# Kernel optimization log

Hardware: AMD Instinct MI355X
Metric: run time of the kernel (lower is better)

## Reference

```python
import jax, jax.numpy as jnp
import numpy as np

EMBED_DIM = 1024
NUM_HEADS = 16
HEAD_DIM = EMBED_DIM // NUM_HEADS
SCALE = HEAD_DIM ** -0.5
EPS = 1e-5


def _layer_norm(x, w, b):
    mu = jnp.mean(x, axis=-1, keepdims=True)
    var = jnp.mean(jnp.square(x - mu), axis=-1, keepdims=True)
    return (x - mu) * jax.lax.rsqrt(var + EPS) * w + b


def setup_inputs() -> dict:
    key = jax.random.key(0)
    ks = jax.random.split(key, 8)
    B, L, Lp, C = 8, 4096, 256, EMBED_DIM
    gain = 0.05  # xavier_uniform gain
    lim = gain * np.sqrt(6.0 / (C + C))
    return {
        "prompt": jax.random.normal(ks[0], (B, Lp, C), jnp.float32),
        "x": jax.random.normal(ks[1], (B, L, C), jnp.float32),
        "ln_q_w": jnp.ones((C,), jnp.float32),
        "ln_q_b": jnp.zeros((C,), jnp.float32),
        "ln_k_w": jnp.ones((C,), jnp.float32),
        "ln_k_b": jnp.zeros((C,), jnp.float32),
        "Wq": jax.random.uniform(ks[2], (C, C), jnp.float32, -lim, lim),
        "bq": jnp.zeros((C,), jnp.float32),
        "Wk": jax.random.uniform(ks[3], (C, C), jnp.float32, -lim, lim),
        "bk": jnp.zeros((C,), jnp.float32),
        "Wo": jax.random.uniform(ks[4], (C, C), jnp.float32, -lim, lim),
        "bo": jnp.zeros((C,), jnp.float32),
        "alpha": jnp.asarray(0.5, jnp.float32),
    }


def reference(prompt, x, ln_q_w, ln_q_b, ln_k_w, ln_k_b, Wq, bq, Wk, bk, Wo, bo, alpha):
    B, L, C = x.shape
    Lp = prompt.shape[1]
    H, D = NUM_HEADS, HEAD_DIM

    q = _layer_norm(prompt, ln_q_w, ln_q_b)
    k = _layer_norm(x, ln_k_w, ln_k_b)

    # torch Linear: y = x @ W^T + b (W is [out, in])
    Q = (q @ Wq.T + bq).reshape(B, Lp, H, D).transpose(0, 2, 1, 3)  # [B,H,Lp,D]
    K = (k @ Wk.T + bk).reshape(B, L, H, D).transpose(0, 2, 1, 3)   # [B,H,L,D]
    V = x.reshape(B, L, H, D).transpose(0, 2, 1, 3)                  # [B,H,L,D]

    Q = jnp.clip(Q, -10.0, 10.0)
    K = jnp.clip(K, -10.0, 10.0)

    scores = jnp.einsum('bhqd,bhkd->bhqk', Q, K) * SCALE
    scores = scores - jax.lax.stop_gradient(jnp.max(scores, axis=-1, keepdims=True))
    attn = jax.nn.softmax(scores, axis=-1)

    attn_out = jnp.einsum('bhqk,bhkd->bhqd', attn, V)
    attn_out = attn_out.transpose(0, 2, 1, 3).reshape(B, Lp, C)
    attn_out = attn_out @ Wo.T + bo

    global_signal = jnp.mean(attn_out, axis=1, keepdims=True)  # [B,1,C]
    a = jax.nn.sigmoid(alpha) * 0.3
    return x + a * global_signal
```

## Files before the change

### kernel.cpp

```cpp
#include <hip/hip_runtime.h>

typedef __attribute__((ext_vector_type(8))) short  short8;
typedef __attribute__((ext_vector_type(4))) float  floatx4;
typedef __attribute__((ext_vector_type(2))) unsigned int uint2v;

#define NS 8

__device__ __forceinline__ unsigned short f2b(float f) {
  union { float f; unsigned u; } c; c.f = f;
  unsigned r = c.u + 0x7FFFu + ((c.u >> 16) & 1u);
  return (unsigned short)(r >> 16);
}

__device__ __forceinline__ float b2f(unsigned short u) {
  union { unsigned u; float f; } c; c.u = (unsigned)u << 16;
  return c.f;
}

__device__ __forceinline__ unsigned cvt_pk_bf16(float a, float b) {
  unsigned r;
  asm("v_cvt_pk_bf16_f32 %0, %1, %2" : "=v"(r) : "v"(a), "v"(b));
  return r;
}

__device__ __forceinline__ void async_copy16(const void* g, void* l) {
  __builtin_amdgcn_global_load_lds(
      (const __attribute__((address_space(1))) void*)g,
      (__attribute__((address_space(3))) void*)l, 16, 0, 0);
}

__global__ __launch_bounds__(256) void ln_bf16_kernel(
    const float* __restrict__ src, const float* __restrict__ w,
    const float* __restrict__ bias, unsigned short* __restrict__ dst) {
  const size_t row = blockIdx.x;
  const int t = threadIdx.x;
  const float4 v = *(const float4*)&src[row * 1024 + t * 4];
  float s = v.x + v.y + v.z + v.w;
  float q = v.x * v.x + v.y * v.y + v.z * v.z + v.w * v.w;
#pragma unroll
  for (int m = 32; m >= 1; m >>= 1) {
    s += __shfl_xor(s, m, 64);
    q += __shfl_xor(q, m, 64);
  }
  __shared__ float ss[4], sq[4];
  if ((t & 63) == 0) { ss[t >> 6] = s; sq[t >> 6] = q; }
  __syncthreads();
  s = ss[0] + ss[1] + ss[2] + ss[3];
  q = sq[0] + sq[1] + sq[2] + sq[3];
  const float mu = s * (1.f / 1024.f);
  const float var = q * (1.f / 1024.f) - mu * mu;
  const float rs = rsqrtf(var + 1e-5f);
  const float4 wv = *(const float4*)&w[t * 4];
  const float4 bv = *(const float4*)&bias[t * 4];
  ushort4 o;
  o.x = f2b((v.x - mu) * rs * wv.x + bv.x);
  o.y = f2b((v.y - mu) * rs * wv.y + bv.y);
  o.z = f2b((v.z - mu) * rs * wv.z + bv.z);
  o.w = f2b((v.w - mu) * rs * wv.w + bv.w);
  *(ushort4*)&dst[row * 1024 + t * 4] = o;
}

__global__ __launch_bounds__(256) void conv_bf16_kernel(
    const float* __restrict__ src, unsigned short* __restrict__ dst) {
  const size_t i = (size_t)blockIdx.x * 256 + threadIdx.x;
  const float4 v = ((const float4*)src)[i];
  ushort4 o;
  o.x = f2b(v.x); o.y = f2b(v.y); o.z = f2b(v.z); o.w = f2b(v.w);
  ((ushort4*)dst)[i] = o;
}

__global__ __launch_bounds__(256) void vtrans_kernel(
    const float* __restrict__ x, unsigned short* __restrict__ Vbf) {
  const int bh = blockIdx.x, kb = blockIdx.y;
  const int b = bh >> 4, h = bh & 15;
  const int t = threadIdx.x;
  const int d = t >> 2, kc = t & 3;
  const float* xp = x + (size_t)(b * 4096 + kb * 256) * 1024 + h * 64 + d;
  unsigned short* vp = Vbf + ((size_t)bh * 64 + d) * 4096 + kb * 256;
#pragma unroll
  for (int c = 0; c < 8; c++) {
    const int kk = c * 32 + kc * 8;
    short8 o;
#pragma unroll
    for (int j = 0; j < 8; j++)
      o[j] = (short)f2b(xp[(size_t)(kk + j) * 1024]);
    *(short8*)&vp[kk] = o;
  }
}

__global__ __launch_bounds__(256) void gemm_bt_kernel(
    const unsigned short* __restrict__ A, const unsigned short* __restrict__ W,
    const float* __restrict__ bias, unsigned short* __restrict__ out, int M) {
  __shared__ __align__(16) unsigned short smem[2][128 * 64];
  unsigned short* As = smem[0];
  unsigned short* Bs = smem[1];
  const int tid = threadIdx.x;
  const int wave = tid >> 6, lane = tid & 63;
  const int quad = lane >> 4, l16 = lane & 15;
  const int id = blockIdx.x;
  const size_t m0 = (size_t)(id >> 3) * 128;
  const int n0 = (id & 7) * 128;
  const int wm = (wave >> 1) * 64, wn = (wave & 1) * 64;
  const int r8 = lane >> 3, cvv = lane & 7;
  const int csrc = cvv ^ r8;

  floatx4 acc[4][4];
#pragma unroll
  for (int i = 0; i < 4; i++)
#pragma unroll
    for (int j = 0; j < 4; j++) acc[i][j] = (floatx4){0.f, 0.f, 0.f, 0.f};

  const unsigned short* gA = A + (m0 + wave * 32 + r8) * 1024 + csrc * 8;
  const unsigned short* gB = W + ((size_t)(n0 + wave * 32 + r8)) * 1024 + csrc * 8;

  for (int k0 = 0; k0 < 1024; k0 += 64) {
    __syncthreads();
#pragma unroll
    for (int it = 0; it < 4; ++it) {
      async_copy16(gA + (size_t)it * 8 * 1024 + k0, &As[(wave * 4 + it) * 512]);
      async_copy16(gB + (size_t)it * 8 * 1024 + k0, &Bs[(wave * 4 + it) * 512]);
    }
    __syncthreads();
#pragma unroll
    for (int kh = 0; kh < 2; ++kh) {
      short8 af[4], bf[4];
#pragma unroll
      for (int mi = 0; mi < 4; mi++) {
        int row = wm + mi * 16 + l16;
        af[mi] = *(const short8*)&As[row * 64 + (((kh * 4 + quad) ^ (row & 7)) * 8)];
      }
#pragma unroll
      for (int ni = 0; ni < 4; ni++) {
        int row = wn + ni * 16 + l16;
        bf[ni] = *(const short8*)&Bs[row * 64 + (((kh * 4 + quad) ^ (row & 7)) * 8)];
      }
#pragma unroll
      for (int mi = 0; mi < 4; mi++)
#pragma unroll
        for (int ni = 0; ni < 4; ni++)
          acc[mi][ni] = __builtin_amdgcn_mfma_f32_16x16x32_bf16(af[mi], bf[ni], acc[mi][ni], 0, 0, 0);
    }
  }

  __syncthreads();
  unsigned short* Cs = smem[0];
#pragma unroll
  for (int ni = 0; ni < 4; ni++) {
    int n = n0 + wn + ni * 16 + l16;
    float bv = bias[n];
    int c = wn + ni * 16 + l16;
#pragma unroll
    for (int mi = 0; mi < 4; mi++)
#pragma unroll
      for (int p = 0; p < 4; p++) {
        int r = wm + mi * 16 + quad * 4 + p;
        float v = acc[mi][ni][p] + bv;
        v = fminf(10.f, fmaxf(-10.f, v));
        int cc = c >> 3;
        Cs[r * 128 + ((cc ^ (r & 7)) * 8) + (c & 7)] = f2b(v);
      }
  }
  __syncthreads();
#pragma unroll
  for (int i = 0; i < 8; ++i) {
    int r = (tid >> 4) + 16 * i;
    int cc = tid & 15;
    short8 v = *(const short8*)&Cs[r * 128 + ((cc ^ (r & 7)) * 8)];
    *(short8*)&out[(m0 + r) * 1024 + n0 + cc * 8] = v;
  }
}

__global__ __launch_bounds__(256) void attn_kernel(
    const unsigned short* __restrict__ Qp,
    const unsigned short* __restrict__ Kp,
    const unsigned short* __restrict__ Vbf,
    unsigned short* __restrict__ Onum,
    float* __restrict__ lpart) {
  const int bh = blockIdx.x, split = blockIdx.y;
  const int b = bh >> 4, h = bh & 15;
  const int tid = threadIdx.x, wave = tid >> 6, lane = tid & 63;
  const int quad = lane >> 4, l16 = lane & 15;
  const int r8 = lane >> 3, cvv = lane & 7, csrc = cvv ^ r8;

  __shared__ __align__(16) unsigned short smem[16384];
  unsigned short* Ks = smem;
  unsigned short* Vs = smem + 4096;
  unsigned short* Pw = smem + 8192;

  short8 qf[4][2];
#pragma unroll
  for (int mi = 0; mi < 4; mi++)
#pragma unroll
    for (int kh = 0; kh < 2; kh++)
      qf[mi][kh] = *(const short8*)&Qp[(size_t)(b * 256 + wave * 64 + mi * 16 + l16) * 1024 +
                                       h * 64 + kh * 32 + quad * 8];

  floatx4 oacc[4][4];
  floatx4 lacc[4];
#pragma unroll
  for (int i = 0; i < 4; i++) {
    lacc[i] = (floatx4){0.f, 0.f, 0.f, 0.f};
#pragma unroll
    for (int j = 0; j < 4; j++) oacc[i][j] = (floatx4){0.f, 0.f, 0.f, 0.f};
  }
  short8 ones;
#pragma unroll
  for (int j = 0; j < 8; j++) ones[j] = (short)0x3F80;

  const int kbase = split * (4096 / NS);
  const int rowbase = (wave & 1) * 32;
  const bool isK = (wave < 2);
  const unsigned short* gK = Kp + ((size_t)(b * 4096 + kbase + rowbase + r8)) * 1024 +
                             h * 64 + csrc * 8;
  const unsigned short* gV = Vbf + ((size_t)(bh * 64 + rowbase + r8)) * 4096 +
                             kbase + csrc * 8;

  const int T = 4096 / NS / 64;
  unsigned short* Pb = Pw + wave * 2048;

  uint4 stg[4];
  if (isK) {
#pragma unroll
    for (int it = 0; it < 4; ++it)
      stg[it] = *(const uint4*)&gK[((size_t)it * 8) * 1024];
  } else {
#pragma unroll
    for (int it = 0; it < 4; ++it)
      stg[it] = *(const uint4*)&gV[(size_t)it * 8 * 4096];
  }

  for (int t = 0; t < T; ++t) {
    __syncthreads();
    if (isK) {
#pragma unroll
      for (int it = 0; it < 4; ++it)
        *(uint4*)((char*)Ks + (rowbase + it * 8) * 128 + lane * 16) = stg[it];
    } else {
#pragma unroll
      for (int it = 0; it < 4; ++it)
        *(uint4*)((char*)Vs + (rowbase + it * 8) * 128 + lane * 16) = stg[it];
    }
    __syncthreads();
    if (t + 1 < T) {
      if (isK) {
#pragma unroll
        for (int it = 0; it < 4; ++it)
          stg[it] = *(const uint4*)&gK[((size_t)(t + 1) * 64 + it * 8) * 1024];
      } else {
#pragma unroll
        for (int it = 0; it < 4; ++it)
          stg[it] = *(const uint4*)&gV[(size_t)it * 8 * 4096 + (t + 1) * 64];
      }
    }

#pragma unroll
    for (int mh = 0; mh < 2; ++mh) {
#pragma unroll
      for (int ni = 0; ni < 4; ++ni) {
        const int krow = ni * 16 + l16;
        const short8 kf0 = *(const short8*)&Ks[krow * 64 + ((quad ^ (krow & 7)) * 8)];
        const short8 kf1 = *(const short8*)&Ks[krow * 64 + (((4 + quad) ^ (krow & 7)) * 8)];
#pragma unroll
        for (int m2 = 0; m2 < 2; ++m2) {
          const int mi = mh * 2 + m2;
          floatx4 st = (floatx4){0.f, 0.f, 0.f, 0.f};
          st = __builtin_amdgcn_mfma_f32_16x16x32_bf16(kf0, qf[mi][0], st, 0, 0, 0);
          st = __builtin_amdgcn_mfma_f32_16x16x32_bf16(kf1, qf[mi][1], st, 0, 0, 0);
          const float C = 0.18033688011112042f;
          float e0 = exp2f(st[0] * C);
          float e1 = exp2f(st[1] * C);
          float e2 = exp2f(st[2] * C);
          float e3 = exp2f(st[3] * C);
          unsigned lo = cvt_pk_bf16(e0, e1);
          unsigned hi = cvt_pk_bf16(e2, e3);
          const int qrow = m2 * 16 + l16;
          const int chunk = (ni * 2 + (quad >> 1)) ^ (qrow & 7);
          uint2v wv; wv.x = lo; wv.y = hi;
          *(uint2v*)&Pb[qrow * 64 + chunk * 8 + (quad & 1) * 4] = wv;
        }
      }
#pragma unroll
      for (int kh = 0; kh < 2; ++kh) {
        short8 vf[4];
#pragma unroll
        for (int ni = 0; ni < 4; ni++) {
          int row = ni * 16 + l16;
          vf[ni] = *(const short8*)&Vs[row * 64 + (((kh * 4 + quad) ^ (row & 7)) * 8)];
        }
#pragma unroll
        for (int m2 = 0; m2 < 2; ++m2) {
          const int mi = mh * 2 + m2;
          const int qrow = m2 * 16 + l16;
          short8 pf = *(const short8*)&Pb[qrow * 64 + (((kh * 4 + quad) ^ (qrow & 7)) * 8)];
#pragma unroll
          for (int ni = 0; ni < 4; ni++)
            oacc[mi][ni] = __builtin_amdgcn_mfma_f32_16x16x32_bf16(pf, vf[ni], oacc[mi][ni], 0, 0, 0);
          lacc[mi] = __builtin_amdgcn_mfma_f32_16x16x32_bf16(pf, ones, lacc[mi], 0, 0, 0);
        }
      }
    }
  }

  __syncthreads();
  unsigned short* Cs = smem;
#pragma unroll
  for (int mi = 0; mi < 4; mi++)
#pragma unroll
    for (int ni = 0; ni < 4; ni++)
#pragma unroll
      for (int p = 0; p < 4; p++) {
        int q = wave * 64 + mi * 16 + quad * 4 + p;
        int d = ni * 16 + l16;
        int cc = d >> 3;
        Cs[q * 64 + ((cc ^ (q & 7)) * 8) + (d & 7)] = f2b(oacc[mi][ni][p]);
      }
  __syncthreads();
  unsigned short* Ob = Onum + ((size_t)bh * NS + split) * 256 * 64;
#pragma unroll
  for (int i = 0; i < 8; ++i) {
    int q = (tid >> 3) + 32 * i;
    int cc = tid & 7;
    short8 v = *(const short8*)&Cs[q * 64 + ((cc ^ (q & 7)) * 8)];
    *(short8*)&Ob[q * 64 + cc * 8] = v;
  }
  if (l16 == 0) {
    float* lb = lpart + ((size_t)bh * NS + split) * 256;
#pragma unroll
    for (int mi = 0; mi < 4; mi++)
#pragma unroll
      for (int p = 0; p < 4; p++)
        lb[wave * 64 + mi * 16 + quad * 4 + p] = lacc[mi][p];
  }
}

__global__ __launch_bounds__(256) void reduce_heads_kernel(
    const unsigned short* __restrict__ Onum, const float* __restrict__ lpart,
    float* __restrict__ ho) {
  const int bh = blockIdx.x;
  const int t = threadIdx.x;
  __shared__ float ls[256];
  __shared__ float red[16][64];
  float l = 0.f;
#pragma unroll
  for (int s = 0; s < NS; s++) l += lpart[((size_t)bh * NS + s) * 256 + t];
  ls[t] = l;
  __syncthreads();
  const int d4 = t & 15, qg = t >> 4;
  float4 part = {0.f, 0.f, 0.f, 0.f};
  for (int qi = 0; qi < 16; ++qi) {
    int q = qg * 16 + qi;
    float4 on = {0.f, 0.f, 0.f, 0.f};
#pragma unroll
    for (int s = 0; s < NS; s++) {
      ushort4 v = *(const ushort4*)&Onum[(((size_t)bh * NS + s) * 256 + q) * 64 + d4 * 4];
      on.x += b2f(v.x); on.y += b2f(v.y); on.z += b2f(v.z); on.w += b2f(v.w);
    }
    const float rl = 1.f / ls[q];
    part.x += on.x * rl; part.y += on.y * rl;
    part.z += on.z * rl; part.w += on.w * rl;
  }
  *(float4*)&red[qg][d4 * 4] = part;
  __syncthreads();
  if (t < 64) {
    float v = 0.f;
#pragma unroll
    for (int r = 0; r < 16; ++r) v += red[r][t];
    v *= (1.f / 256.f);
    int b = bh >> 4, h = bh & 15;
    ho[b * 1024 + h * 64 + t] = v;
  }
}

__global__ __launch_bounds__(256) void wo_proj_kernel(
    const float* __restrict__ ho, const float* __restrict__ Wo,
    const float* __restrict__ bo, float* __restrict__ gs) {
  const int b = blockIdx.x >> 2, cg = blockIdx.x & 3;
  const int t = threadIdx.x;
  __shared__ float hs[1024];
#pragma unroll
  for (int i = 0; i < 4; i++) hs[t + i * 256] = ho[b * 1024 + t + i * 256];
  __syncthreads();
  const int c = cg * 256 + t;
  const float* wrow = Wo + (size_t)c * 1024;
  float acc = bo[c];
  for (int k = 0; k < 1024; k += 4) {
    float4 w4 = *(const float4*)&wrow[k];
    acc += w4.x * hs[k] + w4.y * hs[k + 1] + w4.z * hs[k + 2] + w4.w * hs[k + 3];
  }
  gs[b * 1024 + c] = acc;
}

__global__ __launch_bounds__(256) void final_add_kernel(
    const float* __restrict__ x, const float* __restrict__ gs,
    const float* __restrict__ alpha, float* __restrict__ out) {
  const float a = 0.3f / (1.f + __expf(-alpha[0]));
  const size_t i4 = (size_t)blockIdx.x * 256 + threadIdx.x;
  const float4 xv = ((const float4*)x)[i4];
  const float4 g = *(const float4*)&gs[(i4 >> 20) * 1024 + (i4 & 255) * 4];
  float4 o;
  o.x = xv.x + a * g.x; o.y = xv.y + a * g.y;
  o.z = xv.z + a * g.z; o.w = xv.w + a * g.w;
  ((float4*)out)[i4] = o;
}

extern "C" void kernel_launch(void* const* d_in, const int* in_sizes, int n_in,
                              void* d_out, int out_size, void* d_ws, size_t ws_size,
                              hipStream_t stream) {
  const float* prompt = (const float*)d_in[0];
  const float* x      = (const float*)d_in[1];
  const float* lnqw   = (const float*)d_in[2];
  const float* lnqb   = (const float*)d_in[3];
  const float* lnkw   = (const float*)d_in[4];
  const float* lnkb   = (const float*)d_in[5];
  const float* Wq     = (const float*)d_in[6];
  const float* bq     = (const float*)d_in[7];
  const float* Wk     = (const float*)d_in[8];
  const float* bk     = (const float*)d_in[9];
  const float* Wo     = (const float*)d_in[10];
  const float* bo     = (const float*)d_in[11];
  const float* alpha  = (const float*)d_in[12];
  float* out = (float*)d_out;

  char* ws = (char*)d_ws;
  unsigned short* kln = (unsigned short*)(ws + 0);
  unsigned short* Vbf = (unsigned short*)(ws + 0);
  unsigned short* qln = (unsigned short*)(ws + 67108864);
  unsigned short* Wqb = (unsigned short*)(ws + 71303168);
  unsigned short* Wkb = (unsigned short*)(ws + 73400320);
  unsigned short* Qp  = (unsigned short*)(ws + 75497472);
  float* lpart        = (float*)(ws + 79691776);
  float* ho           = (float*)(ws + 80740352);
  float* gs           = (float*)(ws + 80773120);

  char* ob = (char*)d_out;
  unsigned short* Kp   = (unsigned short*)(ob + 0);
  unsigned short* Onum = (unsigned short*)(ob + 67108864);

  ln_bf16_kernel<<<32768, 256, 0, stream>>>(x, lnkw, lnkb, kln);
  ln_bf16_kernel<<<2048, 256, 0, stream>>>(prompt, lnqw, lnqb, qln);
  conv_bf16_kernel<<<1024, 256, 0, stream>>>(Wq, Wqb);
  conv_bf16_kernel<<<1024, 256, 0, stream>>>(Wk, Wkb);
  gemm_bt_kernel<<<128, 256, 0, stream>>>(qln, Wqb, bq, Qp, 2048);
  gemm_bt_kernel<<<2048, 256, 0, stream>>>(kln, Wkb, bk, Kp, 32768);
  vtrans_kernel<<<dim3(128, 16), 256, 0, stream>>>(x, Vbf);
  attn_kernel<<<dim3(128, NS), 256, 0, stream>>>(Qp, Kp, Vbf, Onum, lpart);
  reduce_heads_kernel<<<128, 256, 0, stream>>>(Onum, lpart, ho);
  wo_proj_kernel<<<32, 256, 0, stream>>>(ho, Wo, bo, gs);
  final_add_kernel<<<32768, 256, 0, stream>>>(x, gs, alpha, out);
}
```

Measured before the change: 582.1 us.

## Stage V transpose through LDS and remap GEMM blocks for XCD locality

The V transpose kernel now reads x with coalesced float4 loads into a padded LDS tile and then writes transposed bf16 rows from shared memory. The old version did strided scalar global reads with a 4 KB stride per element. The projection GEMM also remaps block IDs so that consecutive blocks dispatched to the same XCD share M rows, which is meant to improve L2 reuse of A and W. The transpose now uses about 34 KB of LDS and one barrier, and its column reads from the tile may hit bank conflicts.

```diff
diff --git a/kernel.cpp b/kernel.cpp
--- a/kernel.cpp
+++ b/kernel.cpp
@@ -74,17 +74,26 @@
   const int bh = blockIdx.x, kb = blockIdx.y;
   const int b = bh >> 4, h = bh & 15;
   const int t = threadIdx.x;
+  __shared__ __align__(16) unsigned short tile[256][68];
+  const int row16 = t >> 4, c4 = t & 15;
+  const float* xp = x + ((size_t)(b * 4096 + kb * 256 + row16) * 1024) + h * 64 + c4 * 4;
+#pragma unroll
+  for (int pass = 0; pass < 16; ++pass) {
+    const int k = pass * 16 + row16;
+    float4 v = *(const float4*)&xp[(size_t)pass * 16 * 1024];
+    ushort4 o;
+    o.x = f2b(v.x); o.y = f2b(v.y); o.z = f2b(v.z); o.w = f2b(v.w);
+    *(ushort4*)&tile[k][c4 * 4] = o;
+  }
+  __syncthreads();
   const int d = t >> 2, kc = t & 3;
-  const float* xp = x + (size_t)(b * 4096 + kb * 256) * 1024 + h * 64 + d;
-  unsigned short* vp = Vbf + ((size_t)bh * 64 + d) * 4096 + kb * 256;
-#pragma unroll
-  for (int c = 0; c < 8; c++) {
-    const int kk = c * 32 + kc * 8;
+  unsigned short* vp = Vbf + ((size_t)bh * 64 + d) * 4096 + kb * 256 + kc * 64;
+#pragma unroll
+  for (int j = 0; j < 8; ++j) {
     short8 o;
 #pragma unroll
-    for (int j = 0; j < 8; j++)
-      o[j] = (short)f2b(xp[(size_t)(kk + j) * 1024]);
-    *(short8*)&vp[kk] = o;
+    for (int e = 0; e < 8; ++e) o[e] = (short)tile[kc * 64 + j * 8 + e][d];
+    *(short8*)&vp[j * 8] = o;
   }
 }
 
@@ -97,9 +106,10 @@
   const int tid = threadIdx.x;
   const int wave = tid >> 6, lane = tid & 63;
   const int quad = lane >> 4, l16 = lane & 15;
-  const int id = blockIdx.x;
-  const size_t m0 = (size_t)(id >> 3) * 128;
-  const int n0 = (id & 7) * 128;
+  const int chunk = gridDim.x >> 3;
+  const int work = (blockIdx.x & 7) * chunk + (blockIdx.x >> 3);
+  const size_t m0 = (size_t)(work >> 3) * 128;
+  const int n0 = (work & 7) * 128;
   const int wm = (wave >> 1) * 64, wn = (wave & 1) * 64;
   const int r8 = lane >> 3, cvv = lane & 7;
   const int csrc = cvv ^ r8;
```

Result: no change. 581.0 us (-0.2%).
